# Optimization experiments

Hardware: AMD Instinct MI355X
Metric: run time of the kernel (lower is better)

The kernel has to match this reference:

```python
import jax, jax.numpy as jnp
import numpy as np

D_MODEL = 1024
N_HEADS = 16
HEAD_DIM = D_MODEL // N_HEADS


def setup_inputs() -> dict:
    key = jax.random.key(0)
    ks = jax.random.split(key, 12)
    B, S = 2, 2048
    scale = 1.0 / np.sqrt(D_MODEL)
    inp = {
        "query": jax.random.normal(ks[0], (B, S, D_MODEL), jnp.float32),
        "key": jax.random.normal(ks[1], (B, S, D_MODEL), jnp.float32),
        "value": jax.random.normal(ks[2], (B, S, D_MODEL), jnp.float32),
        "Wq": jax.random.normal(ks[3], (D_MODEL, D_MODEL), jnp.float32) * scale,
        "bq": jnp.zeros((D_MODEL,), jnp.float32),
        "Wk": jax.random.normal(ks[4], (D_MODEL, D_MODEL), jnp.float32) * scale,
        "bk": jnp.zeros((D_MODEL,), jnp.float32),
        "Wv": jax.random.normal(ks[5], (D_MODEL, D_MODEL), jnp.float32) * scale,
        "bv": jnp.zeros((D_MODEL,), jnp.float32),
        "Wo": jax.random.normal(ks[6], (D_MODEL, D_MODEL), jnp.float32) * scale,
        "bo": jnp.zeros((D_MODEL,), jnp.float32),
    }
    return inp


def _split_heads(x):
    # [B, S, D] -> [B, H, S, Dh]
    B, S, _ = x.shape
    return x.reshape(B, S, N_HEADS, HEAD_DIM).transpose(0, 2, 1, 3)


def reference(query, key, value, Wq, bq, Wk, bk, Wv, bv, Wo, bo):
    B, S, _ = query.shape
    Q = _split_heads(query @ Wq + bq)   # [B,H,S,Dh]
    K = _split_heads(key @ Wk + bk)
    V = _split_heads(value @ Wv + bv)
    inv_sqrt_dh = 1.0 / np.sqrt(HEAD_DIM).astype(np.float32)
    scores = jnp.einsum("bhqd,bhkd->bhqk", Q, K) * inv_sqrt_dh
    attention = jax.nn.softmax(scores, axis=-1)
    # dropout is identity in eval mode
    out = jnp.einsum("bhqk,bhkd->bhqd", attention, V)
    out = out.transpose(0, 2, 1, 3).reshape(B, S, D_MODEL)
    out = out @ Wo + bo
    return out, attention
```

## Files before the change

kernel.cpp:

```cpp
#include <hip/hip_runtime.h>
#include <math.h>

#define D_MODEL 1024
#define NHEADS 16
#define HDIM 64
#define BATCH 2
#define SEQ 2048
#define MROWS (BATCH * SEQ)

typedef unsigned int uint32;
typedef __attribute__((ext_vector_type(8))) short short8;
typedef __attribute__((ext_vector_type(4))) float f32x4;
typedef __attribute__((ext_vector_type(16))) float f32x16;
typedef __attribute__((ext_vector_type(2))) unsigned int uint2v;

__device__ __forceinline__ unsigned short f2bf(float f) {
  unsigned int u = __float_as_uint(f);
  u += 0x7fffu + ((u >> 16) & 1u);
  return (unsigned short)(u >> 16);
}

__device__ __forceinline__ float fexp2(float x) {
  float r;
  asm("v_exp_f32 %0, %1" : "=v"(r) : "v"(x));
  return r;
}

__device__ __forceinline__ unsigned int cvtpk(float lo, float hi) {
  unsigned int r;
  asm("v_cvt_pk_bf16_f32 %0, %1, %2" : "=v"(r) : "v"(lo), "v"(hi));
  return r;
}

__device__ __forceinline__ void bar_lgkm() {
  asm volatile("s_waitcnt lgkmcnt(0)\n\ts_barrier" ::: "memory");
}

__device__ __forceinline__ void gl_lds16(const void* g, void* l) {
  __builtin_amdgcn_global_load_lds((const __attribute__((address_space(1))) void*)g,
                                   (__attribute__((address_space(3))) void*)l, 16, 0, 0);
}

struct PrepArgs {
  const float* act[3];
  unsigned short* actout[3];
  const float* w[4];
  unsigned short* wout;
};

__global__ __launch_bounds__(256) void prep_kernel(PrepArgs args) {
  int bid = blockIdx.x;
  int t = threadIdx.x;
  if (bid < 6144) {
    int z = bid >> 11, blk = bid & 2047;
    const float* s = args.act[z];
    unsigned short* d = args.actout[z];
    int i = (blk * 256 + t) * 8;
    float4 v0 = *(const float4*)(s + i);
    float4 v1 = *(const float4*)(s + i + 4);
    uint4 o;
    o.x = cvtpk(v0.x, v0.y);
    o.y = cvtpk(v0.z, v0.w);
    o.z = cvtpk(v1.x, v1.y);
    o.w = cvtpk(v1.z, v1.w);
    *(uint4*)(d + i) = o;
  } else {
    __shared__ unsigned short tile[64][80];
    int wb = bid - 6144;
    int zz = wb >> 8, rem = wb & 255;
    int n0 = (rem & 15) * 64, k0 = (rem >> 4) * 64;
    const float* W = args.w[zz];
    unsigned short* WT = args.wout + (size_t)zz * (D_MODEL * D_MODEL);
    int r = t >> 2, cc = (t & 3) * 16;
    const float* src = W + (size_t)(k0 + r) * D_MODEL + n0 + cc;
#pragma unroll
    for (int j = 0; j < 16; j += 4) {
      float4 v = *(const float4*)(src + j);
      tile[r][cc + j + 0] = f2bf(v.x);
      tile[r][cc + j + 1] = f2bf(v.y);
      tile[r][cc + j + 2] = f2bf(v.z);
      tile[r][cc + j + 3] = f2bf(v.w);
    }
    __syncthreads();
    __align__(16) unsigned short tmp[16];
#pragma unroll
    for (int j = 0; j < 16; ++j) tmp[j] = tile[cc + j][r];
    unsigned short* d = WT + (size_t)(n0 + r) * D_MODEL + k0 + cc;
    *(uint4*)d = ((uint4*)tmp)[0];
    *(uint4*)(d + 8) = ((uint4*)tmp)[1];
  }
}

struct GemmArgs {
  const unsigned short* A[3];
  const unsigned short* W[3];
  const float* bias[3];
  void* C[3];
};

__global__ __launch_bounds__(256) void gemm_qkv_kernel(GemmArgs args) {
  int bid = blockIdx.x;
  int wgid = (bid & 7) * 96 + (bid >> 3);
  const unsigned short *A, *WT;
  const float* bias;
  void* C;
  int m0, n0;
  bool vtrans;
  if (wgid < 512) {
    int x = wgid & 7, yz = wgid >> 3, y = yz & 31, z = yz >> 5;
    A = args.A[z]; WT = args.W[z]; bias = args.bias[z]; C = args.C[z];
    n0 = x * 128; m0 = y * 128; vtrans = false;
  } else {
    int w2 = wgid - 512, x2 = w2 & 31, y2 = w2 >> 5;
    A = args.W[2];
    WT = args.A[2];
    bias = args.bias[2]; C = args.C[2];
    n0 = x2 * 128; m0 = y2 * 128; vtrans = true;
  }
  __shared__ __align__(16) unsigned short As[128 * 64];
  __shared__ __align__(16) unsigned short Bs[128 * 64];
  int t = threadIdx.x;
  int wave = t >> 6, lane = t & 63;
  int wm = (wave >> 1) * 64, wn = (wave & 1) * 64;
  int lr = lane & 15, lg = lane >> 4;
  int r8 = lane >> 3, c8 = (lane & 7) * 8;
  f32x4 acc[4][4] = {};

  for (int kt = 0; kt < D_MODEL; kt += 64) {
#pragma unroll
    for (int i = 0; i < 4; ++i) {
      int row = wave * 32 + i * 8;
      gl_lds16(A + (size_t)(m0 + row + r8) * D_MODEL + kt + c8, As + row * 64);
      gl_lds16(WT + (size_t)(n0 + row + r8) * D_MODEL + kt + c8, Bs + row * 64);
    }
    __syncthreads();
    short8 af[4][2], bf[4][2];
#pragma unroll
    for (int f = 0; f < 4; ++f) {
#pragma unroll
      for (int kk = 0; kk < 2; ++kk) {
        af[f][kk] = *(const short8*)((const char*)As + (wm + f * 16 + lr) * 128 + kk * 64 + lg * 16);
        bf[f][kk] = *(const short8*)((const char*)Bs + (wn + f * 16 + lr) * 128 + kk * 64 + lg * 16);
      }
    }
#pragma unroll
    for (int i = 0; i < 4; ++i)
#pragma unroll
      for (int j = 0; j < 4; ++j)
#pragma unroll
        for (int kk = 0; kk < 2; ++kk)
          acc[i][j] = __builtin_amdgcn_mfma_f32_16x16x32_bf16(af[i][kk], bf[j][kk], acc[i][j], 0, 0, 0);
    __syncthreads();
  }
  if (!vtrans) {
#pragma unroll
    for (int i = 0; i < 4; ++i)
#pragma unroll
      for (int j = 0; j < 4; ++j) {
        int col = n0 + wn + j * 16 + lr;
        float bb = bias[col];
#pragma unroll
        for (int r = 0; r < 4; ++r) {
          int row = m0 + wm + i * 16 + lg * 4 + r;
          ((unsigned short*)C)[(size_t)row * D_MODEL + col] = f2bf(acc[i][j][r] + bb);
        }
      }
  } else {
#pragma unroll
    for (int i = 0; i < 4; ++i)
#pragma unroll
      for (int j = 0; j < 4; ++j) {
        int col = n0 + wn + j * 16 + lr;
#pragma unroll
        for (int r = 0; r < 4; ++r) {
          int row = m0 + wm + i * 16 + lg * 4 + r;
          ((unsigned short*)C)[(size_t)row * MROWS + col] = f2bf(acc[i][j][r] + bias[row]);
        }
      }
  }
}

__global__ __launch_bounds__(256) void attn_kernel(const unsigned short* Q, const unsigned short* K,
                                                   const unsigned short* Vt2, float* attn,
                                                   unsigned short* ctx) {
  int bid = blockIdx.x;
  int wgid = (bid & 7) * 64 + (bid >> 3);
  int bh = wgid >> 4;
  int q0 = (wgid & 15) * 128;
  int b = bh >> 4, h = bh & 15;
  int t = threadIdx.x, wave = t >> 6, lane = t & 63;
  int l31 = lane & 31, hi = lane >> 5;

  __shared__ __align__(16) char Ks[2][64 * 128];
  __shared__ __align__(16) char Vs[2][64 * 128];

  const unsigned short* Kp = K + (size_t)(b * SEQ) * D_MODEL + h * HDIM;
  const unsigned short* Vp = Vt2 + (size_t)(h * HDIM) * MROWS + b * SEQ;

  short8 qv[4];
  {
    const unsigned short* qp = Q + (size_t)(b * SEQ + q0 + wave * 32 + l31) * D_MODEL + h * HDIM + hi * 8;
#pragma unroll
    for (int kk = 0; kk < 4; ++kk) qv[kk] = *(const short8*)(qp + kk * 16);
  }

  const float SCL = 0.125f * 1.44269504f;
  float lsum = 0.f;
  f32x16 oacc[2] = {};

#pragma unroll
  for (int c = 0; c < 2; ++c) {
    int idx = t + 256 * c;
    int row = idx >> 3, ch = idx & 7;
    int cb = (ch * 16) ^ ((row & 7) << 4);
    *(uint4*)(Ks[0] + row * 128 + cb) = *(const uint4*)(Kp + (size_t)row * D_MODEL + ch * 8);
    *(uint4*)(Vs[0] + row * 128 + cb) = *(const uint4*)(Vp + (size_t)row * MROWS + ch * 8);
  }
  bar_lgkm();
  int cur = 0;
  for (int ti = 0; ti < 32; ++ti) {
    uint4 nk[2], nv[2];
    bool more = (ti + 1) < 32;
    if (more) {
#pragma unroll
      for (int c = 0; c < 2; ++c) {
        int idx = t + 256 * c;
        int row = idx >> 3, ch = idx & 7;
        nk[c] = *(const uint4*)(Kp + (size_t)((ti + 1) * 64 + row) * D_MODEL + ch * 8);
        nv[c] = *(const uint4*)(Vp + (size_t)row * MROWS + (ti + 1) * 64 + ch * 8);
      }
    }
    f32x16 st[2] = {};
#pragma unroll
    for (int n = 0; n < 2; ++n)
#pragma unroll
      for (int kk = 0; kk < 4; ++kk) {
        int kr = n * 32 + l31;
        short8 ak = *(const short8*)(Ks[cur] + kr * 128 + ((kk * 32 + hi * 16) ^ ((kr & 7) << 4)));
        st[n] = __builtin_amdgcn_mfma_f32_32x32x16_bf16(ak, qv[kk], st[n], 0, 0, 0);
      }
    unsigned int P0[2][4], P1[2][4];
#pragma unroll
    for (int n = 0; n < 2; ++n)
#pragma unroll
      for (int j2 = 0; j2 < 4; ++j2) {
        float p0 = fexp2(st[n][4 * j2 + 0] * SCL);
        float p1 = fexp2(st[n][4 * j2 + 1] * SCL);
        float p2 = fexp2(st[n][4 * j2 + 2] * SCL);
        float p3 = fexp2(st[n][4 * j2 + 3] * SCL);
        lsum += (p0 + p1) + (p2 + p3);
        P0[n][j2] = cvtpk(p0, p1);
        P1[n][j2] = cvtpk(p2, p3);
      }
    short8 pa[4];
#pragma unroll
    for (int n = 0; n < 2; ++n)
#pragma unroll
      for (int c = 0; c < 2; ++c) {
        uint2v s0 = __builtin_amdgcn_permlane32_swap(P0[n][2 * c], P0[n][2 * c + 1], false, false);
        uint2v s1 = __builtin_amdgcn_permlane32_swap(P1[n][2 * c], P1[n][2 * c + 1], false, false);
        uint4 w;
        w.x = s0.x; w.y = s1.x; w.z = s0.y; w.w = s1.y;
        pa[n * 2 + c] = *(short8*)&w;
      }
#pragma unroll
    for (int n2 = 0; n2 < 2; ++n2)
#pragma unroll
      for (int kk = 0; kk < 4; ++kk) {
        int vr = n2 * 32 + l31;
        short8 bv = *(const short8*)(Vs[cur] + vr * 128 + ((kk * 32 + hi * 16) ^ ((vr & 7) << 4)));
        oacc[n2] = __builtin_amdgcn_mfma_f32_32x32x16_bf16(pa[kk], bv, oacc[n2], 0, 0, 0);
      }
    if (more) {
#pragma unroll
      for (int c = 0; c < 2; ++c) {
        int idx = t + 256 * c;
        int row = idx >> 3, ch = idx & 7;
        int cb = (ch * 16) ^ ((row & 7) << 4);
        *(uint4*)(Ks[cur ^ 1] + row * 128 + cb) = nk[c];
        *(uint4*)(Vs[cur ^ 1] + row * 128 + cb) = nv[c];
      }
    }
    bar_lgkm();
    cur ^= 1;
  }
  float tot = lsum + __shfl_xor(lsum, 32, 64);
  float inv = 1.f / tot;
  float iv16[16];
#pragma unroll
  for (int reg = 0; reg < 16; ++reg) {
    int qr = (reg & 3) + 8 * (reg >> 2) + 4 * hi;
    iv16[reg] = __shfl(inv, qr, 64);
  }
#pragma unroll
  for (int n2 = 0; n2 < 2; ++n2)
#pragma unroll
    for (int reg = 0; reg < 16; ++reg) {
      int qr = (reg & 3) + 8 * (reg >> 2) + 4 * hi;
      int row = b * SEQ + q0 + wave * 32 + qr;
      ctx[(size_t)row * D_MODEL + h * HDIM + n2 * 32 + l31] = f2bf(oacc[n2][reg] * iv16[reg]);
    }

  float* rowp[16];
  {
    float* abase = attn + (size_t)bh * SEQ * SEQ + l31;
#pragma unroll
    for (int reg = 0; reg < 16; ++reg) {
      int qr = (reg & 3) + 8 * (reg >> 2) + 4 * hi;
      rowp[reg] = abase + (size_t)(q0 + wave * 32 + qr) * SEQ;
    }
  }
#pragma unroll
  for (int c = 0; c < 2; ++c) {
    int idx = t + 256 * c;
    int row = idx >> 3, ch = idx & 7;
    int cb = (ch * 16) ^ ((row & 7) << 4);
    *(uint4*)(Ks[0] + row * 128 + cb) = *(const uint4*)(Kp + (size_t)row * D_MODEL + ch * 8);
  }
  bar_lgkm();
  cur = 0;
  for (int ti = 0; ti < 32; ++ti) {
    uint4 nk[2];
    bool more = (ti + 1) < 32;
    if (more) {
#pragma unroll
      for (int c = 0; c < 2; ++c) {
        int idx = t + 256 * c;
        int row = idx >> 3, ch = idx & 7;
        nk[c] = *(const uint4*)(Kp + (size_t)((ti + 1) * 64 + row) * D_MODEL + ch * 8);
      }
    }
    f32x16 st[2] = {};
#pragma unroll
    for (int n = 0; n < 2; ++n)
#pragma unroll
      for (int kk = 0; kk < 4; ++kk) {
        int kr = n * 32 + l31;
        short8 bk = *(const short8*)(Ks[cur] + kr * 128 + ((kk * 32 + hi * 16) ^ ((kr & 7) << 4)));
        st[n] = __builtin_amdgcn_mfma_f32_32x32x16_bf16(qv[kk], bk, st[n], 0, 0, 0);
      }
#pragma unroll
    for (int n = 0; n < 2; ++n)
#pragma unroll
      for (int reg = 0; reg < 16; ++reg) {
        float p = fexp2(st[n][reg] * SCL) * iv16[reg];
        __builtin_nontemporal_store(p, rowp[reg] + ti * 64 + n * 32);
      }
    if (more) {
#pragma unroll
      for (int c = 0; c < 2; ++c) {
        int idx = t + 256 * c;
        int row = idx >> 3, ch = idx & 7;
        int cb = (ch * 16) ^ ((row & 7) << 4);
        *(uint4*)(Ks[cur ^ 1] + row * 128 + cb) = nk[c];
      }
    }
    bar_lgkm();
    cur ^= 1;
  }
}

__global__ __launch_bounds__(256) void gemm_o_kernel(const unsigned short* A, const unsigned short* WT,
                                                     const float* bias, float* C) {
  int bid = blockIdx.x;
  int wgid = (bid & 7) * 32 + (bid >> 3);
  int x = wgid & 7, y = wgid >> 3;
  int n0 = x * 128, m0 = y * 128;
  __shared__ __align__(16) unsigned short As[128 * 64];
  __shared__ __align__(16) unsigned short Bs[128 * 64];
  int t = threadIdx.x;
  int wave = t >> 6, lane = t & 63;
  int wm = (wave >> 1) * 64, wn = (wave & 1) * 64;
  int lr = lane & 15, lg = lane >> 4;
  int r8 = lane >> 3, c8 = (lane & 7) * 8;
  f32x4 acc[4][4] = {};

  for (int kt = 0; kt < D_MODEL; kt += 64) {
#pragma unroll
    for (int i = 0; i < 4; ++i) {
      int row = wave * 32 + i * 8;
      gl_lds16(A + (size_t)(m0 + row + r8) * D_MODEL + kt + c8, As + row * 64);
      gl_lds16(WT + (size_t)(n0 + row + r8) * D_MODEL + kt + c8, Bs + row * 64);
    }
    __syncthreads();
    short8 af[4][2], bf[4][2];
#pragma unroll
    for (int f = 0; f < 4; ++f) {
#pragma unroll
      for (int kk = 0; kk < 2; ++kk) {
        af[f][kk] = *(const short8*)((const char*)As + (wm + f * 16 + lr) * 128 + kk * 64 + lg * 16);
        bf[f][kk] = *(const short8*)((const char*)Bs + (wn + f * 16 + lr) * 128 + kk * 64 + lg * 16);
      }
    }
#pragma unroll
    for (int i = 0; i < 4; ++i)
#pragma unroll
      for (int j = 0; j < 4; ++j)
#pragma unroll
        for (int kk = 0; kk < 2; ++kk)
          acc[i][j] = __builtin_amdgcn_mfma_f32_16x16x32_bf16(af[i][kk], bf[j][kk], acc[i][j], 0, 0, 0);
    __syncthreads();
  }
#pragma unroll
  for (int i = 0; i < 4; ++i)
#pragma unroll
    for (int j = 0; j < 4; ++j) {
      int col = n0 + wn + j * 16 + lr;
      float bb = bias[col];
#pragma unroll
      for (int r = 0; r < 4; ++r) {
        int row = m0 + wm + i * 16 + lg * 4 + r;
        C[(size_t)row * D_MODEL + col] = acc[i][j][r] + bb;
      }
    }
}

extern "C" void kernel_launch(void* const* d_in, const int* in_sizes, int n_in,
                              void* d_out, int out_size, void* d_ws, size_t ws_size,
                              hipStream_t stream) {
  const float* query = (const float*)d_in[0];
  const float* key   = (const float*)d_in[1];
  const float* value = (const float*)d_in[2];
  const float* Wq = (const float*)d_in[3];
  const float* bq = (const float*)d_in[4];
  const float* Wk = (const float*)d_in[5];
  const float* bk = (const float*)d_in[6];
  const float* Wv = (const float*)d_in[7];
  const float* bv = (const float*)d_in[8];
  const float* Wo = (const float*)d_in[9];
  const float* bo = (const float*)d_in[10];

  char* ws = (char*)d_ws;
  const size_t MB = (size_t)1 << 20;
  unsigned short* WqT = (unsigned short*)(ws + 0 * MB);
  unsigned short* WvT = (unsigned short*)(ws + 4 * MB);
  unsigned short* WoT = (unsigned short*)(ws + 6 * MB);
  unsigned short* Xq  = (unsigned short*)(ws + 8 * MB);
  unsigned short* Xk  = (unsigned short*)(ws + 16 * MB);
  unsigned short* Xv  = (unsigned short*)(ws + 24 * MB);
  unsigned short* Qw  = (unsigned short*)(ws + 32 * MB);
  unsigned short* Kw  = (unsigned short*)(ws + 40 * MB);
  unsigned short* Vt2 = (unsigned short*)(ws + 48 * MB);
  unsigned short* Cw  = (unsigned short*)(ws + 8 * MB);

  float* out0 = (float*)d_out;
  float* attn = out0 + (size_t)MROWS * D_MODEL;

  PrepArgs pa;
  pa.act[0] = query; pa.act[1] = key; pa.act[2] = value;
  pa.actout[0] = Xq; pa.actout[1] = Xk; pa.actout[2] = Xv;
  pa.w[0] = Wq; pa.w[1] = Wk; pa.w[2] = Wv; pa.w[3] = Wo;
  pa.wout = WqT;
  prep_kernel<<<dim3(7168), 256, 0, stream>>>(pa);

  GemmArgs ga;
  ga.A[0] = Xq; ga.A[1] = Xk; ga.A[2] = Xv;
  ga.W[0] = WqT; ga.W[1] = WqT + (size_t)D_MODEL * D_MODEL; ga.W[2] = WvT;
  ga.bias[0] = bq; ga.bias[1] = bk; ga.bias[2] = bv;
  ga.C[0] = Qw; ga.C[1] = Kw; ga.C[2] = Vt2;
  gemm_qkv_kernel<<<dim3(768), 256, 0, stream>>>(ga);

  attn_kernel<<<dim3(512), 256, 0, stream>>>(Qw, Kw, Vt2, attn, Cw);

  gemm_o_kernel<<<dim3(256), 256, 0, stream>>>(Cw, WoT, bo, out0);
}
```

Baseline: 280.2 us.

## Split attention into context kernel and separate attention-weight writer kernel

The fused attention kernel, which computed the context and then recomputed QK^T to write normalized attention weights, is split in two. The first kernel computes the context and stores each row's inverse softmax denominator to workspace. A second kernel with twice as many blocks, each covering half the key range, recomputes scores and streams out the fp32 attention matrix. This is meant to raise parallelism and occupancy in the write-bound phase, at the cost of an extra launch, reloading Q, and the small invl round-trip through global memory.

```diff
diff --git a/kernel.cpp b/kernel.cpp
--- a/kernel.cpp
+++ b/kernel.cpp
@@ -180,9 +180,9 @@
   }
 }
 
-__global__ __launch_bounds__(256) void attn_kernel(const unsigned short* Q, const unsigned short* K,
-                                                   const unsigned short* Vt2, float* attn,
-                                                   unsigned short* ctx) {
+__global__ __launch_bounds__(256) void attn_ctx_kernel(const unsigned short* Q, const unsigned short* K,
+                                                       const unsigned short* Vt2, float* invl_g,
+                                                       unsigned short* ctx) {
   int bid = blockIdx.x;
   int wgid = (bid & 7) * 64 + (bid >> 3);
   int bh = wgid >> 4;
@@ -286,6 +286,7 @@
   }
   float tot = lsum + __shfl_xor(lsum, 32, 64);
   float inv = 1.f / tot;
+  if (lane < 32) invl_g[(size_t)bh * SEQ + q0 + wave * 32 + l31] = inv;
   float iv16[16];
 #pragma unroll
   for (int reg = 0; reg < 16; ++reg) {
@@ -300,16 +301,37 @@
       int row = b * SEQ + q0 + wave * 32 + qr;
       ctx[(size_t)row * D_MODEL + h * HDIM + n2 * 32 + l31] = f2bf(oacc[n2][reg] * iv16[reg]);
     }
-
-  float* rowp[16];
+}
+
+__global__ __launch_bounds__(256) void attn_w_kernel(const unsigned short* Q, const unsigned short* K,
+                                                     const float* invl_g, float* attn) {
+  int bid = blockIdx.x;
+  int wgid = (bid & 7) * 128 + (bid >> 3);
+  int bh = wgid >> 5;
+  int q0 = ((wgid >> 1) & 15) * 128;
+  int kh = wgid & 1;
+  int b = bh >> 4, h = bh & 15;
+  int t = threadIdx.x, wave = t >> 6, lane = t & 63;
+  int l31 = lane & 31, hi = lane >> 5;
+
+  __shared__ __align__(16) char Ks[2][64 * 128];
+
+  const unsigned short* Kp = K + (size_t)(b * SEQ + kh * 1024) * D_MODEL + h * HDIM;
+
+  short8 qv[4];
   {
-    float* abase = attn + (size_t)bh * SEQ * SEQ + l31;
-#pragma unroll
-    for (int reg = 0; reg < 16; ++reg) {
-      int qr = (reg & 3) + 8 * (reg >> 2) + 4 * hi;
-      rowp[reg] = abase + (size_t)(q0 + wave * 32 + qr) * SEQ;
-    }
-  }
+    const unsigned short* qp = Q + (size_t)(b * SEQ + q0 + wave * 32 + l31) * D_MODEL + h * HDIM + hi * 8;
+#pragma unroll
+    for (int kk = 0; kk < 4; ++kk) qv[kk] = *(const short8*)(qp + kk * 16);
+  }
+  float4 invl4[4];
+#pragma unroll
+  for (int j2 = 0; j2 < 4; ++j2)
+    invl4[j2] = *(const float4*)(invl_g + (size_t)bh * SEQ + q0 + wave * 32 + 8 * j2 + 4 * hi);
+
+  float* abase = attn + (size_t)bh * SEQ * SEQ + (size_t)(q0 + wave * 32 + 4 * hi) * SEQ + kh * 1024 + l31;
+  const float SCL = 0.125f * 1.44269504f;
+
 #pragma unroll
   for (int c = 0; c < 2; ++c) {
     int idx = t + 256 * c;
@@ -318,16 +340,16 @@
     *(uint4*)(Ks[0] + row * 128 + cb) = *(const uint4*)(Kp + (size_t)row * D_MODEL + ch * 8);
   }
   bar_lgkm();
-  cur = 0;
-  for (int ti = 0; ti < 32; ++ti) {
+  int cur = 0;
+  for (int ti2 = 0; ti2 < 16; ++ti2) {
     uint4 nk[2];
-    bool more = (ti + 1) < 32;
+    bool more = (ti2 + 1) < 16;
     if (more) {
 #pragma unroll
       for (int c = 0; c < 2; ++c) {
         int idx = t + 256 * c;
         int row = idx >> 3, ch = idx & 7;
-        nk[c] = *(const uint4*)(Kp + (size_t)((ti + 1) * 64 + row) * D_MODEL + ch * 8);
+        nk[c] = *(const uint4*)(Kp + (size_t)((ti2 + 1) * 64 + row) * D_MODEL + ch * 8);
       }
     }
     f32x16 st[2] = {};
@@ -339,12 +361,13 @@
         short8 bk = *(const short8*)(Ks[cur] + kr * 128 + ((kk * 32 + hi * 16) ^ ((kr & 7) << 4)));
         st[n] = __builtin_amdgcn_mfma_f32_32x32x16_bf16(qv[kk], bk, st[n], 0, 0, 0);
       }
+    float* tb = abase + ti2 * 64;
 #pragma unroll
     for (int n = 0; n < 2; ++n)
 #pragma unroll
       for (int reg = 0; reg < 16; ++reg) {
-        float p = fexp2(st[n][reg] * SCL) * iv16[reg];
-        __builtin_nontemporal_store(p, rowp[reg] + ti * 64 + n * 32);
+        float p = fexp2(st[n][reg] * SCL) * invl4[reg >> 2][reg & 3];
+        __builtin_nontemporal_store(p, tb + (size_t)((reg & 3) + 8 * (reg >> 2)) * SEQ + n * 32);
       }
     if (more) {
 #pragma unroll
@@ -442,6 +465,7 @@
   unsigned short* Kw  = (unsigned short*)(ws + 40 * MB);
   unsigned short* Vt2 = (unsigned short*)(ws + 48 * MB);
   unsigned short* Cw  = (unsigned short*)(ws + 8 * MB);
+  float* invl_g       = (float*)(ws + 16 * MB);
 
   float* out0 = (float*)d_out;
   float* attn = out0 + (size_t)MROWS * D_MODEL;
@@ -460,7 +484,8 @@
   ga.C[0] = Qw; ga.C[1] = Kw; ga.C[2] = Vt2;
   gemm_qkv_kernel<<<dim3(768), 256, 0, stream>>>(ga);
 
-  attn_kernel<<<dim3(512), 256, 0, stream>>>(Qw, Kw, Vt2, attn, Cw);
+  attn_ctx_kernel<<<dim3(512), 256, 0, stream>>>(Qw, Kw, Vt2, invl_g, Cw);
+  attn_w_kernel<<<dim3(1024), 256, 0, stream>>>(Qw, Kw, invl_g, attn);
 
   gemm_o_kernel<<<dim3(256), 256, 0, stream>>>(Cw, WoT, bo, out0);
 }
```

After: 290.9 us. +3.8%, slower.
